# Optimization experiments

Measured on AMD Instinct MI355X. Metric: run time of the kernel, lower is better.

The kernel has to match this reference:

```python
import jax, jax.numpy as jnp
import numpy as np

UNITS = 1024
OMEGA = np.float32(2.0 * np.pi / UNITS)  # Hopf rotation frequency tied to units
MU = np.float32(1.0)                      # bifurcation parameter (the stop-gradient ones)


def _hopf_act(z_prev, z_i):
    # Hopf normal-form activation: z_i + ((mu - |z_i|^2) + i*omega) * z_i
    r2 = z_i.real * z_i.real + z_i.imag * z_i.imag  # float32 [B,U]
    coef = jax.lax.complex(MU - r2, jnp.full_like(r2, OMEGA))
    return z_i + coef * z_i


def setup_inputs() -> dict:
    key = jax.random.key(0)
    ks = jax.random.split(key, 8)
    B, T, U = 64, 512, UNITS
    ws = np.float32(1.0 / np.sqrt(2.0 * U))  # glorot-ish scale for complex weights
    return {
        "x_real": jax.random.normal(ks[0], (B, T, U), dtype=jnp.float32),
        "x_imag": jax.random.normal(ks[1], (B, T, U), dtype=jnp.float32),
        "A_real": jax.random.normal(ks[2], (U, U), dtype=jnp.float32) * ws,
        "A_imag": jax.random.normal(ks[3], (U, U), dtype=jnp.float32) * ws,
        "B_real": jax.random.normal(ks[4], (U, U), dtype=jnp.float32) * ws,
        "B_imag": jax.random.normal(ks[5], (U, U), dtype=jnp.float32) * ws,
        "z0_real": jax.random.normal(ks[6], (B, U), dtype=jnp.float32) * 0.1,
        "z0_imag": jax.random.normal(ks[7], (B, U), dtype=jnp.float32) * 0.1,
    }


def reference(x_real, x_imag, A_real, A_imag, B_real, B_imag, z0_real, z0_imag):
    x = jax.lax.complex(x_real, x_imag)      # [B,T,U] complex64
    A = jax.lax.complex(A_real, A_imag)      # [U,U]
    Bw = jax.lax.complex(B_real, B_imag)     # [U,U]
    z0 = jax.lax.complex(z0_real, z0_imag)   # [B,U]

    def step(z, x_t):
        # z_i = (z @ A + x @ B) / 2 ; new state is z_i, output is Hopf activation
        z_i = (jnp.matmul(z, A) + jnp.matmul(x_t, Bw)) * np.complex64(0.5)
        y_t = _hopf_act(z, z_i)
        return z_i, y_t

    xs = jnp.swapaxes(x, 0, 1)               # [T,B,U]
    _, ys = jax.lax.scan(step, z0, xs)       # ys: [T,B,U]
    ys = jnp.swapaxes(ys, 0, 1)              # [B,T,U]
    # return real/imag stacked so output is float32 [B,T,U,2]
    return jnp.stack([ys.real, ys.imag], axis=-1)
```

## Files before the change

kernel.cpp:

```cpp
#include <hip/hip_runtime.h>
#include <hip/hip_bf16.h>


#define U_DIM 1024
#define T_STEPS 512
#define B_DIM 64
#define CHUNK 16
#define NCH 32

typedef __bf16 bf16;
typedef __attribute__((ext_vector_type(8))) __bf16 bf16x8;
typedef __attribute__((ext_vector_type(4))) float floatx4;
typedef __attribute__((ext_vector_type(8))) float floatx8;
typedef __attribute__((ext_vector_type(2))) float floatx2;
typedef __attribute__((ext_vector_type(4))) int intx4;

static constexpr float OMEGA_F = 0.006135923151542565f;

__global__ __launch_bounds__(256) void wtrans_kernel(
    const float* __restrict__ a0, const float* __restrict__ a1,
    const float* __restrict__ a2, const float* __restrict__ a3,
    bf16* __restrict__ d0, bf16* __restrict__ d1,
    bf16* __restrict__ d2, bf16* __restrict__ d3)
{
  __shared__ bf16 tile[32][33];
  const float* src;
  bf16* dst;
  switch (blockIdx.z) {
    case 0: src = a0; dst = d0; break;
    case 1: src = a1; dst = d1; break;
    case 2: src = a2; dst = d2; break;
    default: src = a3; dst = d3; break;
  }
  const int tx = threadIdx.x;
  const int ty = threadIdx.y;
  const int k0 = blockIdx.x * 32;
  const int n0 = blockIdx.y * 32;
#pragma unroll
  for (int i = 0; i < 4; ++i) {
    int k = k0 + ty + i * 8;
    tile[ty + i * 8][tx] = (bf16)(0.5f * src[(size_t)k * U_DIM + n0 + tx]);
  }
  __syncthreads();
#pragma unroll
  for (int i = 0; i < 4; ++i) {
    int n = n0 + ty + i * 8;
    dst[(size_t)n * U_DIM + k0 + tx] = tile[tx][ty + i * 8];
  }
}

__global__ __launch_bounds__(256) void zinit2_kernel(
    const float* __restrict__ zr, const float* __restrict__ zi,
    bf16* __restrict__ br, bf16* __restrict__ bi)
{
  size_t idx = (size_t)blockIdx.x * 256 + threadIdx.x;
  int row = (int)(idx >> 10);
  int col = (int)(idx & 1023);
  float vr = 0.f, vi = 0.f;
  if (row < 128) {
    int b = row & 63;
    vr = zr[(size_t)b * U_DIM + col];
    vi = zi[(size_t)b * U_DIM + col];
  }
  br[idx] = (bf16)vr;
  bi[idx] = (bf16)vi;
}

__global__ __launch_bounds__(256, 2) void phase1_kernel(
    const float* __restrict__ Xr, const float* __restrict__ Xi,
    const bf16* __restrict__ Wr, const bf16* __restrict__ Wi,
    float* __restrict__ out)
{
  __shared__ __align__(16) bf16 ldsA[2][4][128][8];
  __shared__ __align__(16) bf16 ldsB[2][4][128][8];

  const int t = threadIdx.x;
  const int lane = t & 63;
  const int wave = t >> 6;
  const int wm = wave >> 1;
  const int wn = wave & 1;
  const int n0 = blockIdx.x * 128;
  const int m0 = blockIdx.y * 128;
  const int l16 = lane & 15;
  const int kqf = lane >> 4;

  const int sm = t & 127;
  const int skq = t >> 7;

  floatx4 accr[4][4], acci[4][4];
#pragma unroll
  for (int ms = 0; ms < 4; ++ms)
#pragma unroll
    for (int ns = 0; ns < 4; ++ns) {
      accr[ms][ns] = (floatx4){0.f, 0.f, 0.f, 0.f};
      acci[ms][ns] = (floatx4){0.f, 0.f, 0.f, 0.f};
    }

  const float* xr_base = Xr + (size_t)(m0 + sm) * U_DIM;
  const float* xi_base = Xi + (size_t)(m0 + sm) * U_DIM;
  const bf16* wr_base = Wr + (size_t)(n0 + sm) * U_DIM;
  const bf16* wi_base = Wi + (size_t)(n0 + sm) * U_DIM;

  floatx8 pxr[2], pxi[2];
  bf16x8 pwr[2], pwi[2];

#define P1_LOADS(KB)                                        \
  do {                                                      \
    int ko0 = (KB) + skq * 8;                               \
    int ko1 = ko0 + 16;                                     \
    pxr[0] = *(const floatx8*)(xr_base + ko0);              \
    pxi[0] = *(const floatx8*)(xi_base + ko0);              \
    pwr[0] = *(const bf16x8*)(wr_base + ko0);               \
    pwi[0] = *(const bf16x8*)(wi_base + ko0);               \
    pxr[1] = *(const floatx8*)(xr_base + ko1);              \
    pxi[1] = *(const floatx8*)(xi_base + ko1);              \
    pwr[1] = *(const bf16x8*)(wr_base + ko1);               \
    pwi[1] = *(const bf16x8*)(wi_base + ko1);               \
  } while (0)

  P1_LOADS(0);

#pragma unroll 1
  for (int kb = 0; kb < U_DIM; kb += 32) {
    *(bf16x8*)&ldsA[0][skq][sm][0]     = __builtin_convertvector(pxr[0], bf16x8);
    *(bf16x8*)&ldsA[1][skq][sm][0]     = __builtin_convertvector(pxi[0], bf16x8);
    *(bf16x8*)&ldsB[0][skq][sm][0]     = pwr[0];
    *(bf16x8*)&ldsB[1][skq][sm][0]     = pwi[0];
    *(bf16x8*)&ldsA[0][skq + 2][sm][0] = __builtin_convertvector(pxr[1], bf16x8);
    *(bf16x8*)&ldsA[1][skq + 2][sm][0] = __builtin_convertvector(pxi[1], bf16x8);
    *(bf16x8*)&ldsB[0][skq + 2][sm][0] = pwr[1];
    *(bf16x8*)&ldsB[1][skq + 2][sm][0] = pwi[1];
    __syncthreads();

    if (kb + 32 < U_DIM) P1_LOADS(kb + 32);

    bf16x8 br_[4], bi_[4];
#pragma unroll
    for (int ns = 0; ns < 4; ++ns) {
      int nrow = wn * 64 + ns * 16 + l16;
      br_[ns] = *(const bf16x8*)&ldsB[0][kqf][nrow][0];
      bi_[ns] = *(const bf16x8*)&ldsB[1][kqf][nrow][0];
    }
#pragma unroll
    for (int ms = 0; ms < 4; ++ms) {
      int mrow = wm * 64 + ms * 16 + l16;
      bf16x8 a_r = *(const bf16x8*)&ldsA[0][kqf][mrow][0];
      bf16x8 a_i = *(const bf16x8*)&ldsA[1][kqf][mrow][0];
      intx4 v = __builtin_bit_cast(intx4, a_i);
      v = v ^ (int)0x80008000u;
      bf16x8 n_ai = __builtin_bit_cast(bf16x8, v);
#pragma unroll
      for (int ns = 0; ns < 4; ++ns) {
        accr[ms][ns] = __builtin_amdgcn_mfma_f32_16x16x32_bf16(a_r,  br_[ns], accr[ms][ns], 0, 0, 0);
        accr[ms][ns] = __builtin_amdgcn_mfma_f32_16x16x32_bf16(n_ai, bi_[ns], accr[ms][ns], 0, 0, 0);
        acci[ms][ns] = __builtin_amdgcn_mfma_f32_16x16x32_bf16(a_r,  bi_[ns], acci[ms][ns], 0, 0, 0);
        acci[ms][ns] = __builtin_amdgcn_mfma_f32_16x16x32_bf16(a_i,  br_[ns], acci[ms][ns], 0, 0, 0);
      }
    }
    __syncthreads();
  }
#undef P1_LOADS

  const int rb = (lane >> 4) * 4;
#pragma unroll
  for (int ms = 0; ms < 4; ++ms)
#pragma unroll
    for (int ns = 0; ns < 4; ++ns)
#pragma unroll
      for (int r = 0; r < 4; ++r) {
        int row = m0 + wm * 64 + ms * 16 + rb + r;
        int col = n0 + wn * 64 + ns * 16 + l16;
        floatx2 v = {accr[ms][ns][r], acci[ms][ns][r]};
        *(floatx2*)(out + ((size_t)row * U_DIM + col) * 2) = v;
      }
}

__global__ __launch_bounds__(256, 3) void bigstep_kernel(
    const bf16* __restrict__ Zr_in, const bf16* __restrict__ Zi_in,
    const bf16* __restrict__ Wr, const bf16* __restrict__ Wi,
    bf16* __restrict__ Zr_out, bf16* __restrict__ Zi_out,
    float* __restrict__ out, int s, int write_y)
{
  __shared__ floatx2 hs[3][32 * 64];

  const int lane = threadIdx.x & 63;
  const int wave = threadIdx.x >> 6;
  const int n0 = blockIdx.x * 64;
  const int m0 = blockIdx.y * 32;
  const int l16 = lane & 15;
  const int kq = (lane >> 4) * 8;
  const int kbase = wave * 256;

  floatx4 accr[2][4], acci[2][4];
#pragma unroll
  for (int ms = 0; ms < 2; ++ms)
#pragma unroll
    for (int ns = 0; ns < 4; ++ns) {
      accr[ms][ns] = (floatx4){0.f, 0.f, 0.f, 0.f};
      acci[ms][ns] = (floatx4){0.f, 0.f, 0.f, 0.f};
    }

  const bf16* zr0 = Zr_in + (size_t)(m0 + l16) * U_DIM + kbase + kq;
  const bf16* zi0 = Zi_in + (size_t)(m0 + l16) * U_DIM + kbase + kq;
  const bf16* wr0 = Wr + (size_t)(n0 + l16) * U_DIM + kbase + kq;
  const bf16* wi0 = Wi + (size_t)(n0 + l16) * U_DIM + kbase + kq;

#pragma unroll 2
  for (int kb = 0; kb < 256; kb += 32) {
    bf16x8 ar[2], ai[2], nai[2];
#pragma unroll
    for (int ms = 0; ms < 2; ++ms) {
      ar[ms] = *(const bf16x8*)(zr0 + (size_t)ms * 16 * U_DIM + kb);
      ai[ms] = *(const bf16x8*)(zi0 + (size_t)ms * 16 * U_DIM + kb);
      intx4 v = __builtin_bit_cast(intx4, ai[ms]);
      v = v ^ (int)0x80008000u;
      nai[ms] = __builtin_bit_cast(bf16x8, v);
    }
    bf16x8 br[4], bi[4];
#pragma unroll
    for (int ns = 0; ns < 4; ++ns) {
      br[ns] = *(const bf16x8*)(wr0 + (size_t)ns * 16 * U_DIM + kb);
      bi[ns] = *(const bf16x8*)(wi0 + (size_t)ns * 16 * U_DIM + kb);
    }
#pragma unroll
    for (int ms = 0; ms < 2; ++ms)
#pragma unroll
      for (int ns = 0; ns < 4; ++ns) {
        accr[ms][ns] = __builtin_amdgcn_mfma_f32_16x16x32_bf16(ar[ms], br[ns], accr[ms][ns], 0, 0, 0);
        accr[ms][ns] = __builtin_amdgcn_mfma_f32_16x16x32_bf16(nai[ms], bi[ns], accr[ms][ns], 0, 0, 0);
        acci[ms][ns] = __builtin_amdgcn_mfma_f32_16x16x32_bf16(ar[ms], bi[ns], acci[ms][ns], 0, 0, 0);
        acci[ms][ns] = __builtin_amdgcn_mfma_f32_16x16x32_bf16(ai[ms], br[ns], acci[ms][ns], 0, 0, 0);
      }
  }

  const int rb = (lane >> 4) * 4;
  if (wave != 0) {
#pragma unroll
    for (int ms = 0; ms < 2; ++ms)
#pragma unroll
      for (int ns = 0; ns < 4; ++ns)
#pragma unroll
        for (int r = 0; r < 4; ++r) {
          int rl = ms * 16 + rb + r;
          int cl = ns * 16 + l16;
          hs[wave - 1][rl * 64 + cl] = (floatx2){accr[ms][ns][r], acci[ms][ns][r]};
        }
  }
  __syncthreads();
  if (wave == 0) {
#pragma unroll
    for (int ms = 0; ms < 2; ++ms)
#pragma unroll
      for (int ns = 0; ns < 4; ++ns)
#pragma unroll
        for (int r = 0; r < 4; ++r) {
          int rl = ms * 16 + rb + r;
          int cl = ns * 16 + l16;
          int idx = rl * 64 + cl;
          floatx2 p0 = hs[0][idx];
          floatx2 p1 = hs[1][idx];
          floatx2 p2 = hs[2][idx];
          int row = m0 + rl;
          int c = row >> 6;
          int b = row & 63;
          int tt = c * CHUNK + s;
          int col = n0 + cl;
          size_t o = (((size_t)b * T_STEPS + tt) * U_DIM + col) * 2;
          floatx2 u = *(const floatx2*)(out + o);
          float zrv = accr[ms][ns][r] + p0.x + p1.x + p2.x + u.x;
          float ziv = acci[ms][ns][r] + p0.y + p1.y + p2.y + u.y;
          Zr_out[(size_t)row * U_DIM + col] = (bf16)zrv;
          Zi_out[(size_t)row * U_DIM + col] = (bf16)ziv;
          if (write_y) {
            float r2 = zrv * zrv + ziv * ziv;
            float cr = 2.0f - r2;
            floatx2 y = {cr * zrv - OMEGA_F * ziv, cr * ziv + OMEGA_F * zrv};
            *(floatx2*)(out + o) = y;
          }
        }
  }
}

extern "C" void kernel_launch(void* const* d_in, const int* in_sizes, int n_in,
                              void* d_out, int out_size, void* d_ws, size_t ws_size,
                              hipStream_t stream)
{
  const float* Xr  = (const float*)d_in[0];
  const float* Xi  = (const float*)d_in[1];
  const float* Ar  = (const float*)d_in[2];
  const float* Ai  = (const float*)d_in[3];
  const float* Br  = (const float*)d_in[4];
  const float* Bi  = (const float*)d_in[5];
  const float* z0r = (const float*)d_in[6];
  const float* z0i = (const float*)d_in[7];
  float* out = (float*)d_out;

  char* ws = (char*)d_ws;
  const size_t WW = (size_t)U_DIM * U_DIM;
  const size_t SB = (size_t)(1 + NCH) * B_DIM * U_DIM;
  const size_t CHOFF = (size_t)B_DIM * U_DIM;
  bf16* Atr = (bf16*)ws;
  bf16* Ati = Atr + WW;
  bf16* Btr = Ati + WW;
  bf16* Bti = Btr + WW;
  bf16* S0r = Bti + WW;
  bf16* S0i = S0r + SB;
  bf16* S1r = S0i + SB;
  bf16* S1i = S1r + SB;

  (void)in_sizes; (void)n_in; (void)out_size; (void)ws_size;

  wtrans_kernel<<<dim3(32, 32, 4), dim3(32, 8), 0, stream>>>(
      Ar, Ai, Br, Bi, Atr, Ati, Btr, Bti);

  zinit2_kernel<<<dim3((unsigned)(SB / 256)), dim3(256), 0, stream>>>(
      z0r, z0i, S0r, S0i);

  phase1_kernel<<<dim3(8, 256), dim3(256), 0, stream>>>(Xr, Xi, Btr, Bti, out);

  for (int s = 0; s < CHUNK; ++s) {
    const bf16 *ir_, *ii_;
    bf16 *or_, *oi_;
    if ((s & 1) == 0) { ir_ = S0r + CHOFF; ii_ = S0i + CHOFF; or_ = S1r + CHOFF; oi_ = S1i + CHOFF; }
    else              { ir_ = S1r + CHOFF; ii_ = S1i + CHOFF; or_ = S0r + CHOFF; oi_ = S0i + CHOFF; }
    bigstep_kernel<<<dim3(16, 64), dim3(256), 0, stream>>>(
        ir_, ii_, Atr, Ati, or_, oi_, out, s, 0);
  }

  for (int s = 0; s < CHUNK; ++s) {
    const bf16 *ir_, *ii_;
    bf16 *or_, *oi_;
    if (s == 0)       { ir_ = S0r;         ii_ = S0i;         or_ = S1r + CHOFF; oi_ = S1i + CHOFF; }
    else if (s & 1)   { ir_ = S1r + CHOFF; ii_ = S1i + CHOFF; or_ = S0r + CHOFF; oi_ = S0i + CHOFF; }
    else              { ir_ = S0r + CHOFF; ii_ = S0i + CHOFF; or_ = S1r + CHOFF; oi_ = S1i + CHOFF; }
    bigstep_kernel<<<dim3(16, 64), dim3(256), 0, stream>>>(
        ir_, ii_, Atr, Ati, or_, oi_, out, s, 1);
  }
}
```

Measured before the change: 3.610 ms.

## Restructure recurrence step kernel to single-wave tiles and skip zero-state chunk step

The per-step bigstep kernel becomes single-wave 32x32 tiles that each run the full K loop, with an XCD-aware tile mapping. This removes the LDS split-K reduction and the __syncthreads. The first step for the non-initial chunks, whose input state is zero, is now a plain copy of the precomputed input projection, and the matmul for it runs only on the first chunk. Phase1 uses a flattened 1D grid with higher occupancy bounds, and zinit shrinks to just the needed rows. The trade-off is smaller tiles, so each wave does more redundant global loads of the weights.

```diff
diff --git a/kernel.cpp b/kernel.cpp
--- a/kernel.cpp
+++ b/kernel.cpp
@@ -56,17 +56,26 @@
   size_t idx = (size_t)blockIdx.x * 256 + threadIdx.x;
   int row = (int)(idx >> 10);
   int col = (int)(idx & 1023);
-  float vr = 0.f, vi = 0.f;
-  if (row < 128) {
-    int b = row & 63;
-    vr = zr[(size_t)b * U_DIM + col];
-    vi = zi[(size_t)b * U_DIM + col];
-  }
-  br[idx] = (bf16)vr;
-  bi[idx] = (bf16)vi;
-}
-
-__global__ __launch_bounds__(256, 2) void phase1_kernel(
+  int b = row & 63;
+  br[idx] = (bf16)zr[(size_t)b * U_DIM + col];
+  bi[idx] = (bf16)zi[(size_t)b * U_DIM + col];
+}
+
+__global__ __launch_bounds__(256) void step0copy_kernel(
+    const float* __restrict__ u, bf16* __restrict__ S1r, bf16* __restrict__ S1i)
+{
+  size_t idx = (size_t)blockIdx.x * 256 + threadIdx.x;
+  int row = 64 + (int)(idx >> 10);
+  int col = (int)(idx & 1023);
+  int c = row >> 6;
+  int b = row & 63;
+  int t = c * CHUNK;
+  floatx2 v = *(const floatx2*)(u + (((size_t)b * T_STEPS + t) * U_DIM + col) * 2);
+  S1r[(size_t)row * U_DIM + col] = (bf16)v.x;
+  S1i[(size_t)row * U_DIM + col] = (bf16)v.y;
+}
+
+__global__ __launch_bounds__(256, 4) void phase1_kernel(
     const float* __restrict__ Xr, const float* __restrict__ Xi,
     const bf16* __restrict__ Wr, const bf16* __restrict__ Wi,
     float* __restrict__ out)
@@ -79,8 +88,8 @@
   const int wave = t >> 6;
   const int wm = wave >> 1;
   const int wn = wave & 1;
-  const int n0 = blockIdx.x * 128;
-  const int m0 = blockIdx.y * 128;
+  const int n0 = (blockIdx.x & 7) * 128;
+  const int m0 = (blockIdx.x >> 3) * 128;
   const int l16 = lane & 15;
   const int kqf = lane >> 4;
 
@@ -175,38 +184,44 @@
       }
 }
 
-__global__ __launch_bounds__(256, 3) void bigstep_kernel(
+__global__ __launch_bounds__(64) void bigstep_kernel(
     const bf16* __restrict__ Zr_in, const bf16* __restrict__ Zi_in,
     const bf16* __restrict__ Wr, const bf16* __restrict__ Wi,
     bf16* __restrict__ Zr_out, bf16* __restrict__ Zi_out,
     float* __restrict__ out, int s, int write_y)
 {
-  __shared__ floatx2 hs[3][32 * 64];
-
-  const int lane = threadIdx.x & 63;
-  const int wave = threadIdx.x >> 6;
-  const int n0 = blockIdx.x * 64;
-  const int m0 = blockIdx.y * 32;
+  const int lane = threadIdx.x;
+  const int l = blockIdx.x;
+  int n_tile, m_tile;
+  if (gridDim.x == 2048) {
+    int xcd = l & 7, j = l >> 3;
+    n_tile = xcd * 4 + (j & 3);
+    m_tile = j >> 2;
+  } else {
+    n_tile = l & 31;
+    m_tile = l >> 5;
+  }
+  const int n0 = n_tile * 32;
+  const int m0 = m_tile * 32;
   const int l16 = lane & 15;
   const int kq = (lane >> 4) * 8;
-  const int kbase = wave * 256;
-
-  floatx4 accr[2][4], acci[2][4];
+
+  floatx4 accr[2][2], acci[2][2];
 #pragma unroll
   for (int ms = 0; ms < 2; ++ms)
 #pragma unroll
-    for (int ns = 0; ns < 4; ++ns) {
+    for (int ns = 0; ns < 2; ++ns) {
       accr[ms][ns] = (floatx4){0.f, 0.f, 0.f, 0.f};
       acci[ms][ns] = (floatx4){0.f, 0.f, 0.f, 0.f};
     }
 
-  const bf16* zr0 = Zr_in + (size_t)(m0 + l16) * U_DIM + kbase + kq;
-  const bf16* zi0 = Zi_in + (size_t)(m0 + l16) * U_DIM + kbase + kq;
-  const bf16* wr0 = Wr + (size_t)(n0 + l16) * U_DIM + kbase + kq;
-  const bf16* wi0 = Wi + (size_t)(n0 + l16) * U_DIM + kbase + kq;
-
-#pragma unroll 2
-  for (int kb = 0; kb < 256; kb += 32) {
+  const bf16* zr0 = Zr_in + (size_t)(m0 + l16) * U_DIM + kq;
+  const bf16* zi0 = Zi_in + (size_t)(m0 + l16) * U_DIM + kq;
+  const bf16* wr0 = Wr + (size_t)(n0 + l16) * U_DIM + kq;
+  const bf16* wi0 = Wi + (size_t)(n0 + l16) * U_DIM + kq;
+
+#pragma unroll 4
+  for (int kb = 0; kb < U_DIM; kb += 32) {
     bf16x8 ar[2], ai[2], nai[2];
 #pragma unroll
     for (int ms = 0; ms < 2; ++ms) {
@@ -216,16 +231,16 @@
       v = v ^ (int)0x80008000u;
       nai[ms] = __builtin_bit_cast(bf16x8, v);
     }
-    bf16x8 br[4], bi[4];
-#pragma unroll
-    for (int ns = 0; ns < 4; ++ns) {
+    bf16x8 br[2], bi[2];
+#pragma unroll
+    for (int ns = 0; ns < 2; ++ns) {
       br[ns] = *(const bf16x8*)(wr0 + (size_t)ns * 16 * U_DIM + kb);
       bi[ns] = *(const bf16x8*)(wi0 + (size_t)ns * 16 * U_DIM + kb);
     }
 #pragma unroll
     for (int ms = 0; ms < 2; ++ms)
 #pragma unroll
-      for (int ns = 0; ns < 4; ++ns) {
+      for (int ns = 0; ns < 2; ++ns) {
         accr[ms][ns] = __builtin_amdgcn_mfma_f32_16x16x32_bf16(ar[ms], br[ns], accr[ms][ns], 0, 0, 0);
         accr[ms][ns] = __builtin_amdgcn_mfma_f32_16x16x32_bf16(nai[ms], bi[ns], accr[ms][ns], 0, 0, 0);
         acci[ms][ns] = __builtin_amdgcn_mfma_f32_16x16x32_bf16(ar[ms], bi[ns], acci[ms][ns], 0, 0, 0);
@@ -234,51 +249,30 @@
   }
 
   const int rb = (lane >> 4) * 4;
-  if (wave != 0) {
-#pragma unroll
-    for (int ms = 0; ms < 2; ++ms)
-#pragma unroll
-      for (int ns = 0; ns < 4; ++ns)
-#pragma unroll
-        for (int r = 0; r < 4; ++r) {
-          int rl = ms * 16 + rb + r;
-          int cl = ns * 16 + l16;
-          hs[wave - 1][rl * 64 + cl] = (floatx2){accr[ms][ns][r], acci[ms][ns][r]};
+#pragma unroll
+  for (int ms = 0; ms < 2; ++ms)
+#pragma unroll
+    for (int ns = 0; ns < 2; ++ns)
+#pragma unroll
+      for (int r = 0; r < 4; ++r) {
+        int row = m0 + ms * 16 + rb + r;
+        int c = row >> 6;
+        int b = row & 63;
+        int tt = c * CHUNK + s;
+        int col = n0 + ns * 16 + l16;
+        size_t o = (((size_t)b * T_STEPS + tt) * U_DIM + col) * 2;
+        floatx2 u = *(const floatx2*)(out + o);
+        float zrv = accr[ms][ns][r] + u.x;
+        float ziv = acci[ms][ns][r] + u.y;
+        Zr_out[(size_t)row * U_DIM + col] = (bf16)zrv;
+        Zi_out[(size_t)row * U_DIM + col] = (bf16)ziv;
+        if (write_y) {
+          float r2 = zrv * zrv + ziv * ziv;
+          float cr = 2.0f - r2;
+          floatx2 y = {cr * zrv - OMEGA_F * ziv, cr * ziv + OMEGA_F * zrv};
+          *(floatx2*)(out + o) = y;
         }
-  }
-  __syncthreads();
-  if (wave == 0) {
-#pragma unroll
-    for (int ms = 0; ms < 2; ++ms)
-#pragma unroll
-      for (int ns = 0; ns < 4; ++ns)
-#pragma unroll
-        for (int r = 0; r < 4; ++r) {
-          int rl = ms * 16 + rb + r;
-          int cl = ns * 16 + l16;
-          int idx = rl * 64 + cl;
-          floatx2 p0 = hs[0][idx];
-          floatx2 p1 = hs[1][idx];
-          floatx2 p2 = hs[2][idx];
-          int row = m0 + rl;
-          int c = row >> 6;
-          int b = row & 63;
-          int tt = c * CHUNK + s;
-          int col = n0 + cl;
-          size_t o = (((size_t)b * T_STEPS + tt) * U_DIM + col) * 2;
-          floatx2 u = *(const floatx2*)(out + o);
-          float zrv = accr[ms][ns][r] + p0.x + p1.x + p2.x + u.x;
-          float ziv = acci[ms][ns][r] + p0.y + p1.y + p2.y + u.y;
-          Zr_out[(size_t)row * U_DIM + col] = (bf16)zrv;
-          Zi_out[(size_t)row * U_DIM + col] = (bf16)ziv;
-          if (write_y) {
-            float r2 = zrv * zrv + ziv * ziv;
-            float cr = 2.0f - r2;
-            floatx2 y = {cr * zrv - OMEGA_F * ziv, cr * ziv + OMEGA_F * zrv};
-            *(floatx2*)(out + o) = y;
-          }
-        }
-  }
+      }
 }
 
 extern "C" void kernel_launch(void* const* d_in, const int* in_sizes, int n_in,
@@ -313,17 +307,21 @@
   wtrans_kernel<<<dim3(32, 32, 4), dim3(32, 8), 0, stream>>>(
       Ar, Ai, Br, Bi, Atr, Ati, Btr, Bti);
 
-  zinit2_kernel<<<dim3((unsigned)(SB / 256)), dim3(256), 0, stream>>>(
-      z0r, z0i, S0r, S0i);
-
-  phase1_kernel<<<dim3(8, 256), dim3(256), 0, stream>>>(Xr, Xi, Btr, Bti, out);
-
-  for (int s = 0; s < CHUNK; ++s) {
+  zinit2_kernel<<<dim3(512), dim3(256), 0, stream>>>(z0r, z0i, S0r, S0i);
+
+  phase1_kernel<<<dim3(2048), dim3(256), 0, stream>>>(Xr, Xi, Btr, Bti, out);
+
+  step0copy_kernel<<<dim3((unsigned)((2048 - 64) * 4)), dim3(256), 0, stream>>>(
+      out, S1r + CHOFF, S1i + CHOFF);
+  bigstep_kernel<<<dim3(64), dim3(64), 0, stream>>>(
+      S0r + CHOFF, S0i + CHOFF, Atr, Ati, S1r + CHOFF, S1i + CHOFF, out, 0, 0);
+
+  for (int s = 1; s < CHUNK; ++s) {
     const bf16 *ir_, *ii_;
     bf16 *or_, *oi_;
     if ((s & 1) == 0) { ir_ = S0r + CHOFF; ii_ = S0i + CHOFF; or_ = S1r + CHOFF; oi_ = S1i + CHOFF; }
     else              { ir_ = S1r + CHOFF; ii_ = S1i + CHOFF; or_ = S0r + CHOFF; oi_ = S0i + CHOFF; }
-    bigstep_kernel<<<dim3(16, 64), dim3(256), 0, stream>>>(
+    bigstep_kernel<<<dim3(2048), dim3(64), 0, stream>>>(
         ir_, ii_, Atr, Ati, or_, oi_, out, s, 0);
   }
 
@@ -333,7 +331,7 @@
     if (s == 0)       { ir_ = S0r;         ii_ = S0i;         or_ = S1r + CHOFF; oi_ = S1i + CHOFF; }
     else if (s & 1)   { ir_ = S1r + CHOFF; ii_ = S1i + CHOFF; or_ = S0r + CHOFF; oi_ = S0i + CHOFF; }
     else              { ir_ = S0r + CHOFF; ii_ = S0i + CHOFF; or_ = S1r + CHOFF; oi_ = S1i + CHOFF; }
-    bigstep_kernel<<<dim3(16, 64), dim3(256), 0, stream>>>(
+    bigstep_kernel<<<dim3(2048), dim3(64), 0, stream>>>(
         ir_, ii_, Atr, Ati, or_, oi_, out, s, 1);
   }
 }
```

Result: slower. 5.372 ms (+48.8%).
